# Performance work log

Hardware: AMD Instinct MI355X
Metric: run time of the kernel (lower is better)

## Reference

```python
import jax, jax.numpy as jnp
import numpy as np

N_NODES = 40000
N_EDGES = 640000
N_GRAPHS = 64
D_IN = 128
HID = 200
OUT = 2


def _lin(key, fin, fout):
    # torch nn.Linear-style init: U(-1/sqrt(fin), 1/sqrt(fin))
    kw, kb = jax.random.split(key)
    s = 1.0 / np.sqrt(fin)
    W = jax.random.uniform(kw, (fin, fout), jnp.float32, -s, s)
    b = jax.random.uniform(kb, (fout,), jnp.float32, -s, s)
    return W, b


def setup_inputs() -> dict:
    key = jax.random.key(0)
    ks = jax.random.split(key, 10)
    x = jax.random.normal(ks[0], (N_NODES, D_IN), jnp.float32)
    edge_index = jax.random.randint(ks[1], (2, N_EDGES), 0, N_NODES, jnp.int32)
    batch = jnp.sort(jax.random.randint(ks[2], (N_NODES,), 0, N_GRAPHS, jnp.int32))
    W1, b1 = _lin(ks[3], D_IN, HID)
    W2, b2 = _lin(ks[4], HID, HID)
    W3, b3 = _lin(ks[5], HID, HID)
    Wg, bg = _lin(ks[6], HID, HID)
    Wc1, bc1 = _lin(ks[7], HID, HID // 2)
    Wc2, bc2 = _lin(ks[8], HID // 2, OUT)
    return {"x": x, "edge_index": edge_index, "batch": batch,
            "W1": W1, "b1": b1, "W2": W2, "b2": b2, "W3": W3, "b3": b3,
            "Wg": Wg, "bg": bg, "Wc1": Wc1, "bc1": bc1, "Wc2": Wc2, "bc2": bc2}


def reference(x, edge_index, batch, W1, b1, W2, b2, W3, b3, Wg, bg, Wc1, bc1, Wc2, bc2):
    n = x.shape[0]
    # GCNConv with self-loops + symmetric normalization (PyG defaults)
    loop = jnp.arange(n, dtype=edge_index.dtype)
    src = jnp.concatenate([edge_index[0], loop])  # [E+N]
    dst = jnp.concatenate([edge_index[1], loop])
    deg = jax.ops.segment_sum(jnp.ones(src.shape, x.dtype), dst, num_segments=n)
    dinv = jax.lax.rsqrt(jnp.maximum(deg, 1.0))  # deg >= 1 with self-loops
    norm = (dinv[src] * dinv[dst])[:, None]      # [E+N, 1]

    def gcn(h, W, b):
        m = (h @ W)[src] * norm                  # gather + scale per edge
        return jax.ops.segment_sum(m, dst, num_segments=n) + b

    h = jax.nn.relu(gcn(x, W1, b1))
    h = jax.nn.relu(gcn(h, W2, b2))
    h = jax.nn.relu(gcn(h, W3, b3))

    gate = jax.nn.sigmoid(h @ Wg + bg)
    hg = h * gate

    # global_mean_pool over batch assignment
    sums = jax.ops.segment_sum(hg, batch, num_segments=N_GRAPHS)
    cnt = jax.ops.segment_sum(jnp.ones((n,), x.dtype), batch, num_segments=N_GRAPHS)
    pooled = sums / jnp.maximum(cnt, 1.0)[:, None]

    # classifier (dropout is identity in eval)
    hidden = jax.nn.relu(pooled @ Wc1 + bc1)
    logits = hidden @ Wc2 + bc2                  # [N_GRAPHS, 2]
    return logits
```

## Files before the change

kernel.cpp:

```cpp
#include <hip/hip_runtime.h>

#define NG 64
#define HIDW 200
#define DIN 128
#define WKP 224
#define POOL_NC 8

typedef _Float16 half4_t __attribute__((ext_vector_type(4)));
typedef _Float16 half8_t __attribute__((ext_vector_type(8)));
typedef float floatx4 __attribute__((ext_vector_type(4)));


__global__ void build_kernel(const int* __restrict__ dst, int* __restrict__ counts,
                             const int* __restrict__ batch, int* __restrict__ gs,
                             int E, int n) {
  int i = blockIdx.x * 256 + threadIdx.x;
  if (i < E) atomicAdd(&counts[dst[i]], 1);
  if (i < n) {
    int b = batch[i];
    if (i == 0) {
      for (int g = 0; g <= b; ++g) gs[g] = 0;
    } else {
      int bp = batch[i - 1];
      for (int g = bp + 1; g <= b; ++g) gs[g] = i;
    }
    if (i == n - 1) {
      for (int g = b + 1; g <= NG; ++g) gs[g] = n;
    }
  }
}


__global__ __launch_bounds__(256) void scan1_kernel(const int* __restrict__ counts,
                                                    int* __restrict__ blocksum,
                                                    float* __restrict__ dinv, int n) {
  __shared__ int s[256];
  int tid = threadIdx.x;
  int i = blockIdx.x * 256 + tid;
  int c = (i < n) ? counts[i] : 0;
  if (i < n) dinv[i] = rsqrtf((float)(c + 1));
  s[tid] = c;
  __syncthreads();
#pragma unroll
  for (int off = 128; off > 0; off >>= 1) {
    if (tid < off) s[tid] += s[tid + off];
    __syncthreads();
  }
  if (tid == 0) blocksum[blockIdx.x] = s[0];
}


__global__ __launch_bounds__(256) void scan3_kernel(const int* __restrict__ counts,
                                                    const int* __restrict__ blocksum,
                                                    int* __restrict__ row_ptr, int n, int nb) {
  __shared__ int bs[256];
  __shared__ int s[256];
  int tid = threadIdx.x;
  bs[tid] = (tid < blockIdx.x && tid < nb) ? blocksum[tid] : 0;
  __syncthreads();
#pragma unroll
  for (int off = 128; off > 0; off >>= 1) {
    if (tid < off) bs[tid] += bs[tid + off];
    __syncthreads();
  }
  int base = bs[0];

  int i = blockIdx.x * 256 + tid;
  int c = (i < n) ? counts[i] : 0;
  s[tid] = c;
  __syncthreads();
  for (int off = 1; off < 256; off <<= 1) {
    int t = (tid >= off) ? s[tid - off] : 0;
    __syncthreads();
    s[tid] += t;
    __syncthreads();
  }
  if (i < n) row_ptr[i] = base + s[tid] - c;
  if (i == n - 1) row_ptr[n] = base + s[tid];
}

__global__ void fill_kernel(const int* __restrict__ src, const int* __restrict__ dst,
                            const int* __restrict__ row_ptr, int* __restrict__ fill,
                            int* __restrict__ csr_src, int E) {
  int e = blockIdx.x * 256 + threadIdx.x;
  if (e >= E) return;
  int d = dst[e];
  int pos = row_ptr[d] + atomicAdd(&fill[d], 1);
  csr_src[pos] = src[e];
}


__global__ void wprep_kernel(const float* __restrict__ W1, const float* __restrict__ W2,
                             const float* __restrict__ W3, const float* __restrict__ Wg,
                             _Float16* __restrict__ o1, _Float16* __restrict__ o2,
                             _Float16* __restrict__ o3, _Float16* __restrict__ og) {
  int wsel = blockIdx.y;
  const float* W = (wsel == 0) ? W1 : (wsel == 1) ? W2 : (wsel == 2) ? W3 : Wg;
  _Float16* WT = (wsel == 0) ? o1 : (wsel == 1) ? o2 : (wsel == 2) ? o3 : og;
  int K  = (wsel == 0) ? DIN : HIDW;
  int KP = (wsel == 0) ? DIN : WKP;
  int idx = blockIdx.x * 256 + threadIdx.x;
  if (idx >= 256 * KP) return;
  int col = idx / KP, k = idx % KP;
  float v = (col < HIDW && k < K) ? W[(long)k * HIDW + col] : 0.f;
  WT[idx] = (_Float16)v;
}


__global__ void cvt_kernel(const float* __restrict__ x, const float* __restrict__ dinv,
                           _Float16* __restrict__ g0, int n) {
  int t = blockIdx.x * 256 + threadIdx.x;
  if (t >= n * 32) return;
  int node = t >> 5, q = t & 31;
  float di = dinv[node];
  float4 v = *(const float4*)&x[(long)node * 128 + q * 4];
  half4_t r = {(_Float16)(di * v.x), (_Float16)(di * v.y),
               (_Float16)(di * v.z), (_Float16)(di * v.w)};
  ((half4_t*)g0)[(long)node * 32 + q] = r;
}


template <int C>
__global__ __launch_bounds__(256) void agg_kernel(const _Float16* __restrict__ g,
                                                  const int* __restrict__ row_ptr,
                                                  const int* __restrict__ csr_src,
                                                  const float* __restrict__ dinv,
                                                  _Float16* __restrict__ out, int n) {
  int node = blockIdx.x * 4 + (threadIdx.x >> 6);
  int lane = threadIdx.x & 63;
  if (node >= n || lane >= C) return;
  const half4_t* __restrict__ hp = (const half4_t*)g;
  int e0 = row_ptr[node], e1 = row_ptr[node + 1];
  half4_t self = hp[(long)node * C + lane];
  float ax = (float)self.x, ay = (float)self.y;
  float az = (float)self.z, aw = (float)self.w;

  int e = e0;
  for (; e + 16 <= e1; e += 16) {
    int sI[16];
#pragma unroll
    for (int j = 0; j < 16; ++j) sI[j] = csr_src[e + j];
    half4_t vv[16];
#pragma unroll
    for (int j = 0; j < 16; ++j) vv[j] = hp[(long)sI[j] * C + lane];
#pragma unroll
    for (int j = 0; j < 16; ++j) {
      ax += (float)vv[j].x; ay += (float)vv[j].y;
      az += (float)vv[j].z; aw += (float)vv[j].w;
    }
  }
  if (e + 8 <= e1) {
    int sI[8];
#pragma unroll
    for (int j = 0; j < 8; ++j) sI[j] = csr_src[e + j];
    half4_t vv[8];
#pragma unroll
    for (int j = 0; j < 8; ++j) vv[j] = hp[(long)sI[j] * C + lane];
#pragma unroll
    for (int j = 0; j < 8; ++j) {
      ax += (float)vv[j].x; ay += (float)vv[j].y;
      az += (float)vv[j].z; aw += (float)vv[j].w;
    }
    e += 8;
  }
  if (e + 4 <= e1) {
    int sI[4];
#pragma unroll
    for (int j = 0; j < 4; ++j) sI[j] = csr_src[e + j];
    half4_t vv[4];
#pragma unroll
    for (int j = 0; j < 4; ++j) vv[j] = hp[(long)sI[j] * C + lane];
#pragma unroll
    for (int j = 0; j < 4; ++j) {
      ax += (float)vv[j].x; ay += (float)vv[j].y;
      az += (float)vv[j].z; aw += (float)vv[j].w;
    }
    e += 4;
  }
  for (; e < e1; ++e) {
    int s = csr_src[e];
    half4_t v = hp[(long)s * C + lane];
    ax += (float)v.x; ay += (float)v.y; az += (float)v.z; aw += (float)v.w;
  }
  float di = dinv[node];
  half4_t r = {(_Float16)(di * ax), (_Float16)(di * ay),
               (_Float16)(di * az), (_Float16)(di * aw)};
  ((half4_t*)out)[(long)node * C + lane] = r;
}


template <int KP, int AS, int MODE, int DSCALE>
__global__ __launch_bounds__(256, 4) void mgemm_kernel(const _Float16* __restrict__ A,
                                                       const _Float16* __restrict__ WT,
                                                       const float* __restrict__ bias,
                                                       const float* __restrict__ dinv,
                                                       _Float16* __restrict__ out, int N) {
  constexpr int LDK = KP + 8;
  __shared__ _Float16 Bs[64][LDK];
  int tid = threadIdx.x;
  int b = blockIdx.x;
  int strip = (b >> 3) & 3;
  int rg = (b & 7) + 8 * (b >> 5);
  int col0 = strip * 64;

  {
    int c = tid >> 2;
    int ks = (tid & 3) * (KP / 4);
    const _Float16* gw = WT + (long)(col0 + c) * KP + ks;
#pragma unroll
    for (int j = 0; j < KP / 32; ++j)
      *(half8_t*)&Bs[c][ks + j * 8] = *(const half8_t*)(gw + j * 8);
  }
  __syncthreads();

  int lane = tid & 63;
  int wid = tid >> 6;
  int row0 = rg * 128 + wid * 32;
  if (row0 >= N) return;
  int l15 = lane & 15;
  int lq = lane >> 4;

  const _Float16* __restrict__ pa = A + (long)(row0 + l15) * AS + lq * 8;

  floatx4 acc[2][4];
#pragma unroll
  for (int i = 0; i < 2; ++i)
#pragma unroll
    for (int j = 0; j < 4; ++j) acc[i][j] = (floatx4){0.f, 0.f, 0.f, 0.f};

#pragma unroll
  for (int k0 = 0; k0 < KP; k0 += 32) {
    half8_t a[2];
#pragma unroll
    for (int rf = 0; rf < 2; ++rf)
      a[rf] = *(const half8_t*)(pa + (long)rf * 16 * AS + k0);
#pragma unroll
    for (int cf = 0; cf < 4; ++cf) {
      half8_t bv = *(const half8_t*)&Bs[cf * 16 + l15][k0 + lq * 8];
#pragma unroll
      for (int rf = 0; rf < 2; ++rf)
        acc[rf][cf] = __builtin_amdgcn_mfma_f32_16x16x32_f16(a[rf], bv, acc[rf][cf], 0, 0, 0);
    }
  }

#pragma unroll
  for (int cf = 0; cf < 4; ++cf) {
    int col = col0 + cf * 16 + l15;
    if (col >= HIDW) continue;
    float bs = bias[col];
#pragma unroll
    for (int rf = 0; rf < 2; ++rf) {
      int rbase = row0 + rf * 16 + lq * 4;
#pragma unroll
      for (int j = 0; j < 4; ++j) {
        int row = rbase + j;
        float v = acc[rf][cf][j] + bs;
        if (MODE == 1) v = fmaxf(v, 0.f);
        if (MODE == 2) {
          float hv = (float)A[(long)row * AS + col];
          v = hv * (1.f / (1.f + __expf(-v)));
        }
        if (DSCALE) v *= dinv[row];
        out[(long)row * HIDW + col] = (_Float16)v;
      }
    }
  }
}


__global__ __launch_bounds__(256) void pool_partial_kernel(const _Float16* __restrict__ gated,
                                                           const int* __restrict__ gs,
                                                           float* __restrict__ partial, int n) {
  int g = blockIdx.x;
  int c = blockIdx.y;
  int f = threadIdx.x;
  int s = gs[g], e = gs[g + 1];
  int len = e - s;
  int chunk = (len + POOL_NC - 1) / POOL_NC;
  int i0 = s + c * chunk;
  int i1 = i0 + chunk; if (i1 > e) i1 = e;
  if (f < HIDW) {
    float acc = 0.f;
    for (int i = i0; i < i1; ++i) acc += (float)gated[(long)i * HIDW + f];
    partial[(g * POOL_NC + c) * HIDW + f] = acc;
  }
}


__global__ void classifier_kernel(const float* __restrict__ partial,
                                  const int* __restrict__ gs,
                                  const float* __restrict__ Wc1, const float* __restrict__ bc1,
                                  const float* __restrict__ Wc2, const float* __restrict__ bc2,
                                  float* __restrict__ out) {
  int g = blockIdx.x;
  int tid = threadIdx.x;
  __shared__ float pg[HIDW];
  __shared__ float hid[100];
  if (tid < HIDW) {
    float acc = 0.f;
#pragma unroll
    for (int c = 0; c < POOL_NC; ++c) acc += partial[(g * POOL_NC + c) * HIDW + tid];
    float cnt = fmaxf((float)(gs[g + 1] - gs[g]), 1.f);
    pg[tid] = acc / cnt;
  }
  __syncthreads();
  if (tid < 100) {
    float a = bc1[tid];
    for (int k = 0; k < HIDW; ++k) a = fmaf(pg[k], Wc1[k * 100 + tid], a);
    hid[tid] = fmaxf(a, 0.f);
  }
  __syncthreads();
  if (tid < 2) {
    float a = bc2[tid];
    for (int k = 0; k < 100; ++k) a = fmaf(hid[k], Wc2[k * 2 + tid], a);
    out[g * 2 + tid] = a;
  }
}


extern "C" void kernel_launch(void* const* d_in, const int* in_sizes, int n_in,
                              void* d_out, int out_size, void* d_ws, size_t ws_size,
                              hipStream_t stream) {
  const float* x    = (const float*)d_in[0];
  const int*   ei   = (const int*)d_in[1];
  const int*   batch= (const int*)d_in[2];
  const float* W1 = (const float*)d_in[3];  const float* b1 = (const float*)d_in[4];
  const float* W2 = (const float*)d_in[5];  const float* b2 = (const float*)d_in[6];
  const float* W3 = (const float*)d_in[7];  const float* b3 = (const float*)d_in[8];
  const float* Wg = (const float*)d_in[9];  const float* bg = (const float*)d_in[10];
  const float* Wc1= (const float*)d_in[11]; const float* bc1= (const float*)d_in[12];
  const float* Wc2= (const float*)d_in[13]; const float* bc2= (const float*)d_in[14];
  float* out = (float*)d_out;

  const int n = in_sizes[0] / DIN;
  const int E = in_sizes[1] / 2;
  const int* src = ei;
  const int* dst = ei + E;
  const int nb256 = (n + 255) / 256;

  int* counts   = (int*)d_ws;
  int* fill     = counts + n;
  int* row_ptr  = fill + n;
  int* gs       = row_ptr + (n + 4);
  int* blocksum = gs + 68;
  float* dinv   = (float*)(blocksum + 1024);
  int* csr_src  = (int*)(dinv + n);
  float* partial= (float*)(csr_src + E);
  _Float16* wt1 = (_Float16*)(partial + NG * POOL_NC * HIDW);
  _Float16* wt2 = wt1 + 256 * DIN;
  _Float16* wt3 = wt2 + 256 * WKP;
  _Float16* wtg = wt3 + 256 * WKP;
  _Float16* xh   = wtg + 256 * WKP;
  _Float16* bufA = xh + (long)n * DIN;
  _Float16* bufB = bufA + (long)n * HIDW + 64;

  hipMemsetAsync(counts, 0, (size_t)2 * n * sizeof(int), stream);

  dim3 wgrid((256 * WKP + 255) / 256, 4);
  wprep_kernel<<<wgrid, 256, 0, stream>>>(W1, W2, W3, Wg, wt1, wt2, wt3, wtg);

  int eb = (E + 255) / 256;
  build_kernel<<<eb, 256, 0, stream>>>(dst, counts, batch, gs, E, n);
  scan1_kernel<<<nb256, 256, 0, stream>>>(counts, blocksum, dinv, n);
  cvt_kernel<<<(n * 32 + 255) / 256, 256, 0, stream>>>(x, dinv, xh, n);
  scan3_kernel<<<nb256, 256, 0, stream>>>(counts, blocksum, row_ptr, n, nb256);
  fill_kernel<<<eb, 256, 0, stream>>>(src, dst, row_ptr, fill, csr_src, E);

  int ab = (n + 3) / 4;
  int nrg = (n + 127) / 128;
  int gb = ((nrg + 7) / 8) * 8 * 4;

  agg_kernel<32><<<ab, 256, 0, stream>>>(xh, row_ptr, csr_src, dinv, bufA, n);
  mgemm_kernel<DIN, DIN, 1, 1><<<gb, 256, 0, stream>>>(bufA, wt1, b1, dinv, bufB, n);
  agg_kernel<50><<<ab, 256, 0, stream>>>(bufB, row_ptr, csr_src, dinv, bufA, n);
  mgemm_kernel<WKP, HIDW, 1, 1><<<gb, 256, 0, stream>>>(bufA, wt2, b2, dinv, bufB, n);
  agg_kernel<50><<<ab, 256, 0, stream>>>(bufB, row_ptr, csr_src, dinv, bufA, n);
  mgemm_kernel<WKP, HIDW, 1, 0><<<gb, 256, 0, stream>>>(bufA, wt3, b3, dinv, bufB, n);
  mgemm_kernel<WKP, HIDW, 2, 0><<<gb, 256, 0, stream>>>(bufB, wtg, bg, dinv, bufA, n);
  dim3 pgrid(NG, POOL_NC);
  pool_partial_kernel<<<pgrid, 256, 0, stream>>>(bufA, gs, partial, n);
  classifier_kernel<<<NG, 256, 0, stream>>>(partial, gs, Wc1, bc1, Wc2, bc2, out);
}
```

Before: 301.3 us.

## Split edges across half-wavefronts with 16-byte gathers in GCN aggregation

The aggregation kernel now gives each half of a 64-lane wavefront alternate edges of a node and has each lane gather 8 halves (16 bytes) instead of 4. The two halves' partial sums are combined with a cross-lane shuffle, the self-loop term is added at the end, and the result is written with a nontemporal store. Previously 14 of 64 lanes sat idle for the 200-wide layers and each gather was only 8 bytes, so this aims to use more lanes and issue wider memory requests. The weight-prep and graph-build kernels are merged into one launch to save a kernel launch. The cost is an extra shuffle reduction and a serial tail edge handled by one half only.

```diff
diff --git a/kernel.cpp b/kernel.cpp
--- a/kernel.cpp
+++ b/kernel.cpp
@@ -11,22 +11,39 @@
 typedef float floatx4 __attribute__((ext_vector_type(4)));
 
 
-__global__ void build_kernel(const int* __restrict__ dst, int* __restrict__ counts,
-                             const int* __restrict__ batch, int* __restrict__ gs,
-                             int E, int n) {
-  int i = blockIdx.x * 256 + threadIdx.x;
-  if (i < E) atomicAdd(&counts[dst[i]], 1);
-  if (i < n) {
-    int b = batch[i];
-    if (i == 0) {
-      for (int g = 0; g <= b; ++g) gs[g] = 0;
-    } else {
-      int bp = batch[i - 1];
-      for (int g = bp + 1; g <= b; ++g) gs[g] = i;
+__global__ void prep_kernel(const int* __restrict__ dst, int* __restrict__ counts,
+                            const int* __restrict__ batch, int* __restrict__ gs,
+                            int E, int n,
+                            const float* __restrict__ W1, const float* __restrict__ W2,
+                            const float* __restrict__ W3, const float* __restrict__ Wg,
+                            _Float16* __restrict__ o1, _Float16* __restrict__ o2,
+                            _Float16* __restrict__ o3, _Float16* __restrict__ og) {
+  if (blockIdx.y == 0) {
+    int i = blockIdx.x * 256 + threadIdx.x;
+    if (i < E) atomicAdd(&counts[dst[i]], 1);
+    if (i < n) {
+      int b = batch[i];
+      if (i == 0) {
+        for (int g = 0; g <= b; ++g) gs[g] = 0;
+      } else {
+        int bp = batch[i - 1];
+        for (int g = bp + 1; g <= b; ++g) gs[g] = i;
+      }
+      if (i == n - 1) {
+        for (int g = b + 1; g <= NG; ++g) gs[g] = n;
+      }
     }
-    if (i == n - 1) {
-      for (int g = b + 1; g <= NG; ++g) gs[g] = n;
-    }
+  } else {
+    int wsel = blockIdx.y - 1;
+    const float* W = (wsel == 0) ? W1 : (wsel == 1) ? W2 : (wsel == 2) ? W3 : Wg;
+    _Float16* WT = (wsel == 0) ? o1 : (wsel == 1) ? o2 : (wsel == 2) ? o3 : og;
+    int K  = (wsel == 0) ? DIN : HIDW;
+    int KP = (wsel == 0) ? DIN : WKP;
+    int idx = blockIdx.x * 256 + threadIdx.x;
+    if (idx >= 256 * KP) return;
+    int col = idx / KP, k = idx % KP;
+    float v = (col < HIDW && k < K) ? W[(long)k * HIDW + col] : 0.f;
+    WT[idx] = (_Float16)v;
   }
 }
 
@@ -87,23 +104,6 @@
   int d = dst[e];
   int pos = row_ptr[d] + atomicAdd(&fill[d], 1);
   csr_src[pos] = src[e];
-}
-
-
-__global__ void wprep_kernel(const float* __restrict__ W1, const float* __restrict__ W2,
-                             const float* __restrict__ W3, const float* __restrict__ Wg,
-                             _Float16* __restrict__ o1, _Float16* __restrict__ o2,
-                             _Float16* __restrict__ o3, _Float16* __restrict__ og) {
-  int wsel = blockIdx.y;
-  const float* W = (wsel == 0) ? W1 : (wsel == 1) ? W2 : (wsel == 2) ? W3 : Wg;
-  _Float16* WT = (wsel == 0) ? o1 : (wsel == 1) ? o2 : (wsel == 2) ? o3 : og;
-  int K  = (wsel == 0) ? DIN : HIDW;
-  int KP = (wsel == 0) ? DIN : WKP;
-  int idx = blockIdx.x * 256 + threadIdx.x;
-  if (idx >= 256 * KP) return;
-  int col = idx / KP, k = idx % KP;
-  float v = (col < HIDW && k < K) ? W[(long)k * HIDW + col] : 0.f;
-  WT[idx] = (_Float16)v;
 }
 
 
@@ -120,72 +120,73 @@
 }
 
 
-template <int C>
+template <int F>
 __global__ __launch_bounds__(256) void agg_kernel(const _Float16* __restrict__ g,
                                                   const int* __restrict__ row_ptr,
                                                   const int* __restrict__ csr_src,
                                                   const float* __restrict__ dinv,
                                                   _Float16* __restrict__ out, int n) {
   int node = blockIdx.x * 4 + (threadIdx.x >> 6);
+  if (node >= n) return;
   int lane = threadIdx.x & 63;
-  if (node >= n || lane >= C) return;
-  const half4_t* __restrict__ hp = (const half4_t*)g;
+  int esel = lane >> 5;
+  int fl = lane & 31;
+  bool act = fl < F;
+  int flc = act ? fl : 0;
+  const half8_t* __restrict__ hp = (const half8_t*)g;
   int e0 = row_ptr[node], e1 = row_ptr[node + 1];
-  half4_t self = hp[(long)node * C + lane];
-  float ax = (float)self.x, ay = (float)self.y;
-  float az = (float)self.z, aw = (float)self.w;
+  float acc[8] = {0.f, 0.f, 0.f, 0.f, 0.f, 0.f, 0.f, 0.f};
 
   int e = e0;
   for (; e + 16 <= e1; e += 16) {
-    int sI[16];
-#pragma unroll
-    for (int j = 0; j < 16; ++j) sI[j] = csr_src[e + j];
-    half4_t vv[16];
-#pragma unroll
-    for (int j = 0; j < 16; ++j) vv[j] = hp[(long)sI[j] * C + lane];
-#pragma unroll
-    for (int j = 0; j < 16; ++j) {
-      ax += (float)vv[j].x; ay += (float)vv[j].y;
-      az += (float)vv[j].z; aw += (float)vv[j].w;
-    }
+    int sI[8];
+#pragma unroll
+    for (int j = 0; j < 8; ++j) sI[j] = csr_src[e + 2 * j + esel];
+    half8_t vv[8];
+#pragma unroll
+    for (int j = 0; j < 8; ++j) vv[j] = hp[(long)sI[j] * F + flc];
+#pragma unroll
+    for (int j = 0; j < 8; ++j)
+#pragma unroll
+      for (int f = 0; f < 8; ++f) acc[f] += (float)vv[j][f];
   }
   if (e + 8 <= e1) {
-    int sI[8];
-#pragma unroll
-    for (int j = 0; j < 8; ++j) sI[j] = csr_src[e + j];
-    half4_t vv[8];
-#pragma unroll
-    for (int j = 0; j < 8; ++j) vv[j] = hp[(long)sI[j] * C + lane];
-#pragma unroll
-    for (int j = 0; j < 8; ++j) {
-      ax += (float)vv[j].x; ay += (float)vv[j].y;
-      az += (float)vv[j].z; aw += (float)vv[j].w;
-    }
+    int sI[4];
+#pragma unroll
+    for (int j = 0; j < 4; ++j) sI[j] = csr_src[e + 2 * j + esel];
+    half8_t vv[4];
+#pragma unroll
+    for (int j = 0; j < 4; ++j) vv[j] = hp[(long)sI[j] * F + flc];
+#pragma unroll
+    for (int j = 0; j < 4; ++j)
+#pragma unroll
+      for (int f = 0; f < 8; ++f) acc[f] += (float)vv[j][f];
     e += 8;
   }
-  if (e + 4 <= e1) {
-    int sI[4];
-#pragma unroll
-    for (int j = 0; j < 4; ++j) sI[j] = csr_src[e + j];
-    half4_t vv[4];
-#pragma unroll
-    for (int j = 0; j < 4; ++j) vv[j] = hp[(long)sI[j] * C + lane];
-#pragma unroll
-    for (int j = 0; j < 4; ++j) {
-      ax += (float)vv[j].x; ay += (float)vv[j].y;
-      az += (float)vv[j].z; aw += (float)vv[j].w;
-    }
-    e += 4;
-  }
-  for (; e < e1; ++e) {
+  for (; e + 2 <= e1; e += 2) {
+    int s = csr_src[e + esel];
+    half8_t v = hp[(long)s * F + flc];
+#pragma unroll
+    for (int f = 0; f < 8; ++f) acc[f] += (float)v[f];
+  }
+  if (e < e1 && esel == 0) {
     int s = csr_src[e];
-    half4_t v = hp[(long)s * C + lane];
-    ax += (float)v.x; ay += (float)v.y; az += (float)v.z; aw += (float)v.w;
-  }
-  float di = dinv[node];
-  half4_t r = {(_Float16)(di * ax), (_Float16)(di * ay),
-               (_Float16)(di * az), (_Float16)(di * aw)};
-  ((half4_t*)out)[(long)node * C + lane] = r;
+    half8_t v = hp[(long)s * F + flc];
+#pragma unroll
+    for (int f = 0; f < 8; ++f) acc[f] += (float)v[f];
+  }
+
+#pragma unroll
+  for (int f = 0; f < 8; ++f) acc[f] += __shfl_xor(acc[f], 32);
+
+  if (esel == 0 && act) {
+    half8_t self = hp[(long)node * F + fl];
+    float di = dinv[node];
+    half8_t r;
+#pragma unroll
+    for (int f = 0; f < 8; ++f) r[f] = (_Float16)(di * (acc[f] + (float)self[f]));
+    __builtin_nontemporal_store(r, (half8_t*)out + (long)node * F + fl);
+  }
 }
 
 
@@ -351,16 +352,15 @@
   _Float16* wt3 = wt2 + 256 * WKP;
   _Float16* wtg = wt3 + 256 * WKP;
   _Float16* xh   = wtg + 256 * WKP;
-  _Float16* bufA = xh + (long)n * DIN;
-  _Float16* bufB = bufA + (long)n * HIDW + 64;
+  _Float16* bufA = xh + (long)n * DIN + 256;
+  _Float16* bufB = bufA + (long)n * HIDW + 256;
 
   hipMemsetAsync(counts, 0, (size_t)2 * n * sizeof(int), stream);
 
-  dim3 wgrid((256 * WKP + 255) / 256, 4);
-  wprep_kernel<<<wgrid, 256, 0, stream>>>(W1, W2, W3, Wg, wt1, wt2, wt3, wtg);
-
   int eb = (E + 255) / 256;
-  build_kernel<<<eb, 256, 0, stream>>>(dst, counts, batch, gs, E, n);
+  dim3 pgrid0(eb, 5);
+  prep_kernel<<<pgrid0, 256, 0, stream>>>(dst, counts, batch, gs, E, n,
+                                          W1, W2, W3, Wg, wt1, wt2, wt3, wtg);
   scan1_kernel<<<nb256, 256, 0, stream>>>(counts, blocksum, dinv, n);
   cvt_kernel<<<(n * 32 + 255) / 256, 256, 0, stream>>>(x, dinv, xh, n);
   scan3_kernel<<<nb256, 256, 0, stream>>>(counts, blocksum, row_ptr, n, nb256);
@@ -370,11 +370,11 @@
   int nrg = (n + 127) / 128;
   int gb = ((nrg + 7) / 8) * 8 * 4;
 
-  agg_kernel<32><<<ab, 256, 0, stream>>>(xh, row_ptr, csr_src, dinv, bufA, n);
+  agg_kernel<16><<<ab, 256, 0, stream>>>(xh, row_ptr, csr_src, dinv, bufA, n);
   mgemm_kernel<DIN, DIN, 1, 1><<<gb, 256, 0, stream>>>(bufA, wt1, b1, dinv, bufB, n);
-  agg_kernel<50><<<ab, 256, 0, stream>>>(bufB, row_ptr, csr_src, dinv, bufA, n);
+  agg_kernel<25><<<ab, 256, 0, stream>>>(bufB, row_ptr, csr_src, dinv, bufA, n);
   mgemm_kernel<WKP, HIDW, 1, 1><<<gb, 256, 0, stream>>>(bufA, wt2, b2, dinv, bufB, n);
-  agg_kernel<50><<<ab, 256, 0, stream>>>(bufB, row_ptr, csr_src, dinv, bufA, n);
+  agg_kernel<25><<<ab, 256, 0, stream>>>(bufB, row_ptr, csr_src, dinv, bufA, n);
   mgemm_kernel<WKP, HIDW, 1, 0><<<gb, 256, 0, stream>>>(bufA, wt3, b3, dinv, bufB, n);
   mgemm_kernel<WKP, HIDW, 2, 0><<<gb, 256, 0, stream>>>(bufB, wtg, bg, dinv, bufA, n);
   dim3 pgrid(NG, POOL_NC);
```

Measured after the change: 310.2 us. +3.0%, slower.
